# Optimization experiments

Hardware: AMD Instinct MI355X
Metric: run time of the kernel (lower is better)

## Reference

```python
import jax, jax.numpy as jnp
import numpy as np

H = 16  # num_heads


def _rotate_half(t):
    d = t.shape[-1] // 2
    return jnp.concatenate((-t[..., d:], t[..., :d]), axis=-1)


def setup_inputs() -> dict:
    key = jax.random.key(0)
    ks = jax.random.split(key, 4)
    S, HID = 2048, 1280
    D = HID // H  # 80
    x = jax.random.normal(ks[0], (S, HID), dtype=jnp.float32)
    # rotary tables (seq_len, head_dim)
    inv_freq = 1.0 / (10000.0 ** (jnp.arange(0, D, 2, dtype=jnp.float32) / D))
    freqs = jnp.arange(S, dtype=jnp.float32)[:, None] * inv_freq[None, :]  # (S, D/2)
    emb = jnp.concatenate([freqs, freqs], axis=-1)  # (S, D)
    cos = jnp.cos(emb)
    sin = jnp.sin(emb)
    W_qkv = jax.random.normal(ks[1], (HID, 3 * HID), dtype=jnp.float32) * 0.02
    b_qkv = jnp.zeros((3 * HID,), dtype=jnp.float32)
    W_out = jax.random.normal(ks[2], (HID, HID), dtype=jnp.float32) * 0.02
    b_out = jnp.zeros((HID,), dtype=jnp.float32)
    # 8 windows of 256 tokens each -> block-diagonal attention
    cu_seqlens = jnp.arange(0, S + 1, 256, dtype=jnp.int32)  # (9,)
    return {"x": x, "cos": cos, "sin": sin, "W_qkv": W_qkv, "b_qkv": b_qkv,
            "W_out": W_out, "b_out": b_out, "cu_seqlens": cu_seqlens}


def _segment_mask(cu_seqlens, seq_len, dtype):
    positions = jnp.arange(seq_len)
    starts = cu_seqlens[:-1]
    ends = cu_seqlens[1:]
    in_segment = (positions[:, None] >= starts[None, :]) & (positions[:, None] < ends[None, :])
    segment_ids = jnp.argmax(in_segment.astype(jnp.int32), axis=-1)  # (S,)
    same_segment = segment_ids[:, None] == segment_ids[None, :]      # (S, S)
    return jnp.where(same_segment, jnp.zeros((), dtype), jnp.finfo(dtype).min)


def reference(x, cos, sin, W_qkv, b_qkv, W_out, b_out, cu_seqlens):
    S, HID = x.shape
    D = HID // H
    scale = D ** -0.5
    qkv = x @ W_qkv + b_qkv                       # (S, 3*HID)
    q, k, v = jnp.split(qkv, 3, axis=-1)
    q = q.reshape(S, H, D)
    k = k.reshape(S, H, D)
    v = v.reshape(S, H, D)
    cos_f = cos[:, :D][:, None, :]                # (S, 1, D)
    sin_f = sin[:, :D][:, None, :]
    q = q * cos_f + _rotate_half(q) * sin_f       # inline RoPE (fp32)
    k = k * cos_f + _rotate_half(k) * sin_f
    q = jnp.transpose(q, (1, 0, 2))               # (H, S, D)
    k = jnp.transpose(k, (1, 0, 2))
    v = jnp.transpose(v, (1, 0, 2))
    scores = jnp.einsum('hqd,hkd->hqk', q, k) * scale  # (H, S, S)
    mask = _segment_mask(cu_seqlens, S, scores.dtype)  # (S, S) block-diagonal bias
    scores = scores + mask[None, :, :]
    weights = jax.nn.softmax(scores, axis=-1)
    out = jnp.einsum('hqk,hkd->hqd', weights, v)       # (H, S, D)
    out = jnp.transpose(out, (1, 0, 2)).reshape(S, HID)
    return out @ W_out + b_out
```

## Files before the change

### kernel.cpp

```cpp
#include <hip/hip_runtime.h>


typedef short s16x8 __attribute__((ext_vector_type(8)));
typedef __bf16 bf16x8 __attribute__((ext_vector_type(8)));
typedef float f32x4 __attribute__((ext_vector_type(4)));
typedef unsigned short u16;
typedef unsigned long long u64;

__device__ __forceinline__ f32x4 mfma16(s16x8 a, s16x8 b, f32x4 c) {
  return __builtin_amdgcn_mfma_f32_16x16x32_bf16(
      __builtin_bit_cast(bf16x8, a), __builtin_bit_cast(bf16x8, b), c, 0, 0, 0);
}
__device__ __forceinline__ u16 f2b(float f) {
  union { float f; unsigned u; } v;
  v.f = f;
  unsigned r = v.u + 0x7fffu + ((v.u >> 16) & 1u);
  return (u16)(r >> 16);
}
__device__ __forceinline__ void gl16(const u16* g, u16* l) {
  __builtin_amdgcn_global_load_lds(
      (const __attribute__((address_space(1))) unsigned int*)(const void*)g,
      (__attribute__((address_space(3))) unsigned int*)(void*)l, 16, 0, 0);
}

__device__ __forceinline__ void transpose_body(const float* __restrict__ W,
                                               u16* __restrict__ WT, int K, int N,
                                               int nb, int kb, int t, float (*tile)[33]) {
  int tx = t & 31, ty = t >> 5;
#pragma unroll
  for (int r = 0; r < 32; r += 8)
    tile[ty + r][tx] = W[(long)(kb + ty + r) * N + nb + tx];
  __syncthreads();
#pragma unroll
  for (int r = 0; r < 32; r += 8)
    WT[(long)(nb + ty + r) * K + kb + tx] = f2b(tile[tx][ty + r]);
}

__global__ __launch_bounds__(256) void prep(const float* __restrict__ x,
                                            u16* __restrict__ xb,
                                            const float* __restrict__ Wqkv,
                                            u16* __restrict__ WqkvT,
                                            const float* __restrict__ Wout,
                                            u16* __restrict__ WoutT) {
  __shared__ float tile[32][33];
  int bid = blockIdx.x, t = threadIdx.x;
  if (bid < 2560) {
    int i = bid * 256 + t;
    float4 v = ((const float4*)x)[i];
    u64 pk = (u64)f2b(v.x) | ((u64)f2b(v.y) << 16) | ((u64)f2b(v.z) << 32) |
             ((u64)f2b(v.w) << 48);
    ((u64*)xb)[i] = pk;
  } else if (bid < 7360) {
    int i = bid - 2560;
    transpose_body(Wqkv, WqkvT, 1280, 3840, (i % 120) * 32, (i / 120) * 32, t, tile);
  } else {
    int i = bid - 7360;
    transpose_body(Wout, WoutT, 1280, 1280, (i % 40) * 32, (i / 40) * 32, t, tile);
  }
}

__global__ __launch_bounds__(512, 4) void gemm_qkv_rope(const u16* __restrict__ A,
                                                        const u16* __restrict__ B,
                                                        const float* __restrict__ bias,
                                                        const float* __restrict__ cosb,
                                                        const float* __restrict__ sinb,
                                                        u16* __restrict__ Qr,
                                                        u16* __restrict__ Kr,
                                                        u16* __restrict__ VT) {
  __shared__ u16 As[2][128 * 64];
  __shared__ u16 Bs[2][160 * 64];
  const int K = 1280;
  int i = blockIdx.x;
  int xcd = i & 7, j = i >> 3;
  int n0 = (xcd * 3 + (j % 3)) * 160;
  int m0 = (j / 3) * 128;
  int t = threadIdx.x, w = t >> 6, lane = t & 63, lm = lane & 15, quad = lane >> 4;
  int wm = (w >> 1) * 32, wn = (w & 1) * 80;

  const u16* AgSrc[2];
  const u16* BgSrc[3];
#pragma unroll
  for (int c = 0; c < 2; c++) {
    int g = c * 512 + t, row = g >> 3, chp = g & 7;
    AgSrc[c] = A + (long)(m0 + row) * K + ((chp ^ (row & 7)) << 3);
  }
#pragma unroll
  for (int c = 0; c < 2; c++) {
    int g = c * 512 + t, row = g >> 3, chp = g & 7;
    BgSrc[c] = B + (long)(n0 + row) * K + ((chp ^ (row & 7)) << 3);
  }
  {
    int g = 1024 + t, row = g >> 3, chp = g & 7;
    BgSrc[2] = B + (long)(n0 + row) * K + ((chp ^ (row & 7)) << 3);
  }

  auto stage = [&](int buf, int k0) {
#pragma unroll
    for (int c = 0; c < 2; c++) gl16(AgSrc[c] + k0, &As[buf][c * 4096 + w * 512]);
#pragma unroll
    for (int c = 0; c < 2; c++) gl16(BgSrc[c] + k0, &Bs[buf][c * 4096 + w * 512]);
    if (t < 256) gl16(BgSrc[2] + k0, &Bs[buf][8192 + w * 512]);
  };

  f32x4 acc[2][5] = {};
  stage(0, 0);
  stage(1, 64);
  int buf = 0;
  bool low = (t < 256);
  for (int k0 = 0; k0 < K; k0 += 64) {
    if (k0 + 64 < K) {
      if (low) asm volatile("s_waitcnt vmcnt(5)" ::: "memory");
      else     asm volatile("s_waitcnt vmcnt(4)" ::: "memory");
    } else {
      asm volatile("s_waitcnt vmcnt(0)" ::: "memory");
    }
    __builtin_amdgcn_s_barrier();
    asm volatile("" ::: "memory");
#pragma unroll
    for (int kh = 0; kh < 2; kh++) {
      s16x8 af[2], bfr[5];
#pragma unroll
      for (int mt = 0; mt < 2; mt++) {
        int rm = wm + mt * 16 + lm;
        af[mt] = *(const s16x8*)&As[buf][rm * 64 + (((kh * 4 + quad) ^ (rm & 7)) << 3)];
      }
#pragma unroll
      for (int nt = 0; nt < 5; nt++) {
        int rn = wn + nt * 16 + lm;
        bfr[nt] = *(const s16x8*)&Bs[buf][rn * 64 + (((kh * 4 + quad) ^ (rn & 7)) << 3)];
      }
#pragma unroll
      for (int mt = 0; mt < 2; mt++)
#pragma unroll
        for (int nt = 0; nt < 5; nt++)
          acc[mt][nt] = mfma16(af[mt], bfr[nt], acc[mt][nt]);
    }
    asm volatile("" ::: "memory");
    __builtin_amdgcn_s_barrier();
    asm volatile("" ::: "memory");
    if (k0 + 128 < K) stage(buf, k0 + 128);
    buf ^= 1;
  }

  int region = n0 / 1280;
  int hcol = (n0 - region * 1280 + wn) / 80;
  float bv[5];
#pragma unroll
  for (int nt = 0; nt < 5; nt++) bv[nt] = bias[n0 + wn + nt * 16 + lm];

  if (region == 2) {
#pragma unroll
    for (int mt = 0; mt < 2; mt++) {
      int sbase = m0 + wm + mt * 16 + quad * 4;
#pragma unroll
      for (int nt = 0; nt < 5; nt++) {
        int d = nt * 16 + lm;
        u64 pk = 0;
#pragma unroll
        for (int r = 0; r < 4; r++)
          pk |= (u64)f2b(acc[mt][nt][r] + bv[nt]) << (16 * r);
        *(u64*)&VT[((long)hcol * 80 + d) * 2048 + sbase] = pk;
      }
    }
    return;
  }

  const float scale = 0.111803398874989f;
  bool lo = lm < 8;
  u16* Out = (region == 0) ? Qr : Kr;
  float oscale = (region == 0) ? scale : 1.0f;
#pragma unroll
  for (int mt = 0; mt < 2; mt++)
#pragma unroll
    for (int r = 0; r < 4; r++) {
      int s = m0 + wm + mt * 16 + quad * 4 + r;
      float val[5], sw[5];
#pragma unroll
      for (int nt = 0; nt < 5; nt++) val[nt] = acc[mt][nt][r] + bv[nt];
#pragma unroll
      for (int nt = 0; nt < 5; nt++) sw[nt] = __shfl_xor(val[nt], 8);
      float rot[5];
      rot[0] = -(lo ? sw[2] : sw[3]);
      rot[1] = -(lo ? sw[3] : sw[4]);
      rot[2] = lo ? -sw[4] : sw[0];
      rot[3] = lo ? sw[0] : sw[1];
      rot[4] = lo ? sw[1] : sw[2];
      u16* orow = Out + ((long)hcol * 2048 + s) * 80;
      const float* crow = cosb + s * 80;
      const float* srw = sinb + s * 80;
#pragma unroll
      for (int nt = 0; nt < 5; nt++) {
        int d = nt * 16 + lm;
        orow[d] = f2b((val[nt] * crow[d] + rot[nt] * srw[d]) * oscale);
      }
    }
}

__global__ __launch_bounds__(512, 2) void gemm_out(const u16* __restrict__ A,
                                                   const u16* __restrict__ B,
                                                   const float* __restrict__ bias,
                                                   float* __restrict__ C) {
  __shared__ u16 As[2][64 * 64];
  __shared__ u16 Bs[2][160 * 64];
  const int K = 1280;
  int i = blockIdx.x;
  int xcd = i & 7, m0 = (i >> 3) * 64, n0 = xcd * 160;
  int t = threadIdx.x, w = t >> 6, lane = t & 63, lm = lane & 15, quad = lane >> 4;
  int wm = (w >> 1) * 16, wn = (w & 1) * 80;

  const u16* AgSrc;
  {
    int row = t >> 3, chp = t & 7;
    AgSrc = A + (long)(m0 + row) * K + ((chp ^ (row & 7)) << 3);
  }
  const u16* BgSrc[3];
#pragma unroll
  for (int c = 0; c < 2; c++) {
    int g = c * 512 + t, row = g >> 3, chp = g & 7;
    BgSrc[c] = B + (long)(n0 + row) * K + ((chp ^ (row & 7)) << 3);
  }
  {
    int g = 1024 + t, row = g >> 3, chp = g & 7;
    BgSrc[2] = B + (long)(n0 + row) * K + ((chp ^ (row & 7)) << 3);
  }

  auto stage = [&](int buf, int k0) {
    gl16(AgSrc + k0, &As[buf][w * 512]);
#pragma unroll
    for (int c = 0; c < 2; c++) gl16(BgSrc[c] + k0, &Bs[buf][c * 4096 + w * 512]);
    if (t < 256) gl16(BgSrc[2] + k0, &Bs[buf][8192 + w * 512]);
  };

  f32x4 acc[5] = {};
  stage(0, 0);
  int buf = 0;
  for (int k0 = 0; k0 < K; k0 += 64) {
    __syncthreads();
    if (k0 + 64 < K) stage(buf ^ 1, k0 + 64);
#pragma unroll
    for (int kh = 0; kh < 2; kh++) {
      int rm = wm + lm;
      s16x8 af = *(const s16x8*)&As[buf][rm * 64 + (((kh * 4 + quad) ^ (rm & 7)) << 3)];
      s16x8 bfr[5];
#pragma unroll
      for (int nt = 0; nt < 5; nt++) {
        int rn = wn + nt * 16 + lm;
        bfr[nt] = *(const s16x8*)&Bs[buf][rn * 64 + (((kh * 4 + quad) ^ (rn & 7)) << 3)];
      }
#pragma unroll
      for (int nt = 0; nt < 5; nt++) acc[nt] = mfma16(af, bfr[nt], acc[nt]);
    }
    buf ^= 1;
  }
#pragma unroll
  for (int nt = 0; nt < 5; nt++) {
    int col = n0 + wn + nt * 16 + lm;
    float bvv = bias[col];
#pragma unroll
    for (int r = 0; r < 4; r++) {
      int row = m0 + wm + quad * 4 + r;
      C[(long)row * 1280 + col] = acc[nt][r] + bvv;
    }
  }
}

__global__ __launch_bounds__(256, 2) void attn_kernel(const u16* __restrict__ Qr,
                                                      const u16* __restrict__ Kr,
                                                      const u16* __restrict__ VT,
                                                      u16* __restrict__ AO) {
  int qb = blockIdx.x, seg = blockIdx.y, h = blockIdx.z;
  int t = threadIdx.x;
  int w = t >> 6, lane = t & 63, lm = lane & 15, quad = lane >> 4;
  __shared__ u16 Ps[4][16 * 256];

  int s0 = seg * 256 + qb * 64 + w * 16;
  const u16* Qh = Qr + ((long)h * 2048 + s0) * 80;
  const u16* Kh = Kr + ((long)h * 2048 + seg * 256) * 80;

  f32x4 sc[16] = {};
  s16x8 zz = {};
#pragma unroll
  for (int kk = 0; kk < 3; kk++) {
    int dbase = kk * 32 + quad * 8;
    bool valid = dbase < 80;
    s16x8 af = valid ? *(const s16x8*)(Qh + lm * 80 + dbase) : zz;
#pragma unroll
    for (int nt = 0; nt < 16; nt++) {
      s16x8 bfr = valid ? *(const s16x8*)(Kh + (nt * 16 + lm) * 80 + dbase) : zz;
      sc[nt] = mfma16(af, bfr, sc[nt]);
    }
  }

  float rowinv[4];
#pragma unroll
  for (int r = 0; r < 4; r++) {
    float m = sc[0][r];
#pragma unroll
    for (int nt = 1; nt < 16; nt++) m = fmaxf(m, sc[nt][r]);
    m = fmaxf(m, __shfl_xor(m, 1));
    m = fmaxf(m, __shfl_xor(m, 2));
    m = fmaxf(m, __shfl_xor(m, 4));
    m = fmaxf(m, __shfl_xor(m, 8));
    float s = 0.f;
#pragma unroll
    for (int nt = 0; nt < 16; nt++) {
      float e = __expf(sc[nt][r] - m);
      sc[nt][r] = e;
      s += e;
    }
    s += __shfl_xor(s, 1);
    s += __shfl_xor(s, 2);
    s += __shfl_xor(s, 4);
    s += __shfl_xor(s, 8);
    rowinv[r] = 1.0f / s;
    int row = quad * 4 + r;
#pragma unroll
    for (int nt = 0; nt < 16; nt++) {
      int chunk = nt * 2 + (lm >> 3);
      Ps[w][row * 256 + ((chunk ^ row) << 3) + (lm & 7)] = f2b(sc[nt][r]);
    }
  }
  asm volatile("s_waitcnt lgkmcnt(0)" ::: "memory");

  f32x4 oacc[5] = {};
  const u16* Vh = VT + (long)h * 80 * 2048 + seg * 256;
#pragma unroll
  for (int kc = 0; kc < 8; kc++) {
    int row = lm;
    s16x8 pa = *(const s16x8*)&Ps[w][row * 256 + (((kc * 4 + quad) ^ row) << 3)];
#pragma unroll
    for (int nt = 0; nt < 5; nt++) {
      s16x8 bvv = *(const s16x8*)(Vh + (long)(nt * 16 + lm) * 2048 + kc * 32 + quad * 8);
      oacc[nt] = mfma16(pa, bvv, oacc[nt]);
    }
  }
#pragma unroll
  for (int nt = 0; nt < 5; nt++)
#pragma unroll
    for (int r = 0; r < 4; r++)
      AO[(long)(s0 + quad * 4 + r) * 1280 + h * 80 + nt * 16 + lm] =
          f2b(oacc[nt][r] * rowinv[r]);
}

extern "C" void kernel_launch(void* const* d_in, const int* in_sizes, int n_in,
                              void* d_out, int out_size, void* d_ws, size_t ws_size,
                              hipStream_t stream) {
  const float* x    = (const float*)d_in[0];
  const float* cosb = (const float*)d_in[1];
  const float* sinb = (const float*)d_in[2];
  const float* Wqkv = (const float*)d_in[3];
  const float* bqkv = (const float*)d_in[4];
  const float* Wout = (const float*)d_in[5];
  const float* bout = (const float*)d_in[6];

  char* p = (char*)d_ws;
  u16* xb    = (u16*)p;
  u16* WqkvT = (u16*)(p + 5242880);
  u16* WoutT = (u16*)(p + 15073280);
  u16* Qr    = (u16*)(p + 18350080);
  u16* Kr    = (u16*)(p + 23592960);
  u16* VT    = (u16*)(p + 28835840);
  u16* AO    = xb;

  prep<<<dim3(8960), dim3(256), 0, stream>>>(x, xb, Wqkv, WqkvT, Wout, WoutT);
  gemm_qkv_rope<<<dim3(384), dim3(512), 0, stream>>>(xb, WqkvT, bqkv, cosb, sinb,
                                                     Qr, Kr, VT);
  attn_kernel<<<dim3(4, 8, 16), dim3(256), 0, stream>>>(Qr, Kr, VT, AO);
  gemm_out<<<dim3(256), dim3(512), 0, stream>>>(AO, WoutT, bout, (float*)d_out);
}
```

Measured before the change: 162.0 us.

## Split gemm_out into smaller 64x80 tiles with vmcnt-based prefetch pipeline

```diff
diff --git a/kernel.cpp b/kernel.cpp
--- a/kernel.cpp
+++ b/kernel.cpp
@@ -196,47 +196,59 @@
     }
 }
 
-__global__ __launch_bounds__(512, 2) void gemm_out(const u16* __restrict__ A,
+__global__ __launch_bounds__(256, 4) void gemm_out(const u16* __restrict__ A,
                                                    const u16* __restrict__ B,
                                                    const float* __restrict__ bias,
                                                    float* __restrict__ C) {
   __shared__ u16 As[2][64 * 64];
-  __shared__ u16 Bs[2][160 * 64];
+  __shared__ u16 Bs[2][80 * 64];
   const int K = 1280;
   int i = blockIdx.x;
-  int xcd = i & 7, m0 = (i >> 3) * 64, n0 = xcd * 160;
+  int xcd = i & 7;
+  int n0 = xcd * 160 + ((i >> 3) & 1) * 80;
+  int m0 = (i >> 4) * 64;
   int t = threadIdx.x, w = t >> 6, lane = t & 63, lm = lane & 15, quad = lane >> 4;
-  int wm = (w >> 1) * 16, wn = (w & 1) * 80;
-
-  const u16* AgSrc;
+  int wm = w * 16;
+
+  const u16* AgSrc[2];
+  const u16* BgSrc[3];
+#pragma unroll
+  for (int c = 0; c < 2; c++) {
+    int g = c * 256 + t, row = g >> 3, chp = g & 7;
+    AgSrc[c] = A + (long)(m0 + row) * K + ((chp ^ (row & 7)) << 3);
+  }
+#pragma unroll
+  for (int c = 0; c < 2; c++) {
+    int g = c * 256 + t, row = g >> 3, chp = g & 7;
+    BgSrc[c] = B + (long)(n0 + row) * K + ((chp ^ (row & 7)) << 3);
+  }
   {
-    int row = t >> 3, chp = t & 7;
-    AgSrc = A + (long)(m0 + row) * K + ((chp ^ (row & 7)) << 3);
-  }
-  const u16* BgSrc[3];
-#pragma unroll
-  for (int c = 0; c < 2; c++) {
-    int g = c * 512 + t, row = g >> 3, chp = g & 7;
-    BgSrc[c] = B + (long)(n0 + row) * K + ((chp ^ (row & 7)) << 3);
-  }
-  {
-    int g = 1024 + t, row = g >> 3, chp = g & 7;
+    int g = 512 + t, row = g >> 3, chp = g & 7;
     BgSrc[2] = B + (long)(n0 + row) * K + ((chp ^ (row & 7)) << 3);
   }
 
   auto stage = [&](int buf, int k0) {
-    gl16(AgSrc + k0, &As[buf][w * 512]);
-#pragma unroll
-    for (int c = 0; c < 2; c++) gl16(BgSrc[c] + k0, &Bs[buf][c * 4096 + w * 512]);
-    if (t < 256) gl16(BgSrc[2] + k0, &Bs[buf][8192 + w * 512]);
+#pragma unroll
+    for (int c = 0; c < 2; c++) gl16(AgSrc[c] + k0, &As[buf][c * 2048 + w * 512]);
+#pragma unroll
+    for (int c = 0; c < 2; c++) gl16(BgSrc[c] + k0, &Bs[buf][c * 2048 + w * 512]);
+    if (t < 128) gl16(BgSrc[2] + k0, &Bs[buf][4096 + w * 512]);
   };
 
   f32x4 acc[5] = {};
   stage(0, 0);
+  stage(1, 64);
   int buf = 0;
+  bool low = (t < 128);
   for (int k0 = 0; k0 < K; k0 += 64) {
-    __syncthreads();
-    if (k0 + 64 < K) stage(buf ^ 1, k0 + 64);
+    if (k0 + 64 < K) {
+      if (low) asm volatile("s_waitcnt vmcnt(5)" ::: "memory");
+      else     asm volatile("s_waitcnt vmcnt(4)" ::: "memory");
+    } else {
+      asm volatile("s_waitcnt vmcnt(0)" ::: "memory");
+    }
+    __builtin_amdgcn_s_barrier();
+    asm volatile("" ::: "memory");
 #pragma unroll
     for (int kh = 0; kh < 2; kh++) {
       int rm = wm + lm;
@@ -244,17 +256,21 @@
       s16x8 bfr[5];
 #pragma unroll
       for (int nt = 0; nt < 5; nt++) {
-        int rn = wn + nt * 16 + lm;
+        int rn = nt * 16 + lm;
         bfr[nt] = *(const s16x8*)&Bs[buf][rn * 64 + (((kh * 4 + quad) ^ (rn & 7)) << 3)];
       }
 #pragma unroll
       for (int nt = 0; nt < 5; nt++) acc[nt] = mfma16(af, bfr[nt], acc[nt]);
     }
+    asm volatile("" ::: "memory");
+    __builtin_amdgcn_s_barrier();
+    asm volatile("" ::: "memory");
+    if (k0 + 128 < K) stage(buf, k0 + 128);
     buf ^= 1;
   }
 #pragma unroll
   for (int nt = 0; nt < 5; nt++) {
-    int col = n0 + wn + nt * 16 + lm;
+    int col = n0 + nt * 16 + lm;
     float bvv = bias[col];
 #pragma unroll
     for (int r = 0; r < 4; r++) {
@@ -366,5 +382,5 @@
   gemm_qkv_rope<<<dim3(384), dim3(512), 0, stream>>>(xb, WqkvT, bqkv, cosb, sinb,
                                                      Qr, Kr, VT);
   attn_kernel<<<dim3(4, 8, 16), dim3(256), 0, stream>>>(Qr, Kr, VT, AO);
-  gemm_out<<<dim3(256), dim3(512), 0, stream>>>(AO, WoutT, bout, (float*)d_out);
-}
+  gemm_out<<<dim3(512), dim3(256), 0, stream>>>(AO, WoutT, bout, (float*)d_out);
+}
```

Result: no change. 161.6 us (-0.2%).
